# Kernel optimization log

Hardware: AMD Instinct MI355X
Metric: run time of the kernel (lower is better)

Reference implementation:

```python
import jax, jax.numpy as jnp
import numpy as np

N = 50000   # nodes
E = 800000  # edges
D = 128     # nin (= edge_dim)
H = 8       # heads
C = 16      # out_channels per head (nout // nhead)
EPS = 1e-16


def setup_inputs() -> dict:
    key = jax.random.key(0)
    ks = jax.random.split(key, 12)
    s = 1.0 / np.sqrt(D)
    inp = {
        "x": jax.random.normal(ks[0], (N, D), dtype=jnp.float32),
        "edge_attr": jax.random.normal(ks[1], (E, D), dtype=jnp.float32),
        "Wq": jax.random.normal(ks[2], (D, H * C), dtype=jnp.float32) * s,
        "bq": jnp.zeros((H * C,), dtype=jnp.float32),
        "Wk": jax.random.normal(ks[3], (D, H * C), dtype=jnp.float32) * s,
        "bk": jnp.zeros((H * C,), dtype=jnp.float32),
        "Wv": jax.random.normal(ks[4], (D, H * C), dtype=jnp.float32) * s,
        "bv": jnp.zeros((H * C,), dtype=jnp.float32),
        "We": jax.random.normal(ks[5], (D, H * C), dtype=jnp.float32) * s,  # lin_edge, bias=False
        "Wskip": jax.random.normal(ks[6], (D, H * C), dtype=jnp.float32) * s,
        "bskip": jnp.zeros((H * C,), dtype=jnp.float32),
        "edge_index": jax.random.randint(ks[7], (2, E), 0, N, dtype=jnp.int64),
    }
    return inp


def reference(x, edge_attr, Wq, bq, Wk, bk, Wv, bv, We, Wskip, bskip, edge_index):
    src = edge_index[0]  # j (message source)
    dst = edge_index[1]  # i (message target)

    q = (x @ Wq + bq).reshape(N, H, C)           # per-node query
    k = (x @ Wk + bk).reshape(N, H, C)           # per-node key
    v = (x @ Wv + bv).reshape(N, H, C)           # per-node value
    e = (edge_attr @ We).reshape(E, H, C)        # per-edge projection

    q_i = q[dst]                                  # [E, H, C]
    k_j = k[src] + e
    v_j = v[src] + e

    alpha = jnp.einsum("ehc,ehc->eh", q_i, k_j) / np.sqrt(C)  # [E, H]

    # segment softmax over edges grouped by destination node
    m = jax.ops.segment_max(alpha, dst, num_segments=N)        # [N, H]
    m = jnp.where(jnp.isfinite(m), m, 0.0)
    p = jnp.exp(alpha - m[dst])                                # [E, H]
    denom = jax.ops.segment_sum(p, dst, num_segments=N)        # [N, H]
    attn = p / (denom[dst] + EPS)                              # [E, H]

    msg = attn[:, :, None] * v_j                               # [E, H, C]
    out = jax.ops.segment_sum(msg, dst, num_segments=N)        # [N, H, C]
    out = out.reshape(N, H * C)

    # root weight (skip connection)
    out = out + x @ Wskip + bskip
    return out
```

## Files before the change

kernel.cpp:

```cpp
#include <hip/hip_runtime.h>

typedef __attribute__((ext_vector_type(4))) float  f32x4;
typedef __attribute__((ext_vector_type(8))) short  s16x8;

__device__ __forceinline__ short f2bf(float f) {
    unsigned u = __builtin_bit_cast(unsigned, f);
    u += 0x7FFFu + ((u >> 16) & 1u);
    return (short)(u >> 16);
}
__device__ __forceinline__ float bf2f(short s) {
    unsigned u = ((unsigned)(unsigned short)s) << 16;
    return __builtin_bit_cast(float, u);
}

__device__ __forceinline__ void atomic_pk_add_bf16(void* addr, unsigned data) {
    asm volatile("global_atomic_pk_add_bf16 %0, %1, off"
                 :: "v"(addr), "v"(data) : "memory");
}

#define DEPTH 128
#define HEADS 8
#define TILE_M 64

#define LOAD_BFRAG(bfrag, Wt, wc, lane)                                         \
    _Pragma("unroll") for (int nt_ = 0; nt_ < 4; nt_++)                         \
    _Pragma("unroll") for (int kk_ = 0; kk_ < 4; kk_++) {                       \
        int col_ = (wc) + nt_ * 16 + ((lane) & 15);                             \
        int kidx_ = kk_ * 32 + ((lane) >> 4) * 8;                               \
        bfrag[nt_][kk_] = *(const s16x8*)&(Wt)[col_ * 128 + kidx_];             \
    }

__global__ void prep_w(const float* __restrict__ Wq, const float* __restrict__ Wk,
                       const float* __restrict__ Wv, const float* __restrict__ We,
                       const float* __restrict__ Wsk, short* __restrict__ Wt5) {
    int idx = blockIdx.x * 256 + threadIdx.x;
    if (idx >= 5 * DEPTH * DEPTH) return;
    int mat = idx >> 14;
    int rem = idx & 16383;
    int k = rem >> 7, c = rem & 127;
    const float* W = (mat == 0) ? Wq : (mat == 1) ? Wk : (mat == 2) ? Wv : (mat == 3) ? We : Wsk;
    Wt5[mat * 16384 + c * 128 + k] = f2bf(W[k * 128 + c]);
}

__global__ __launch_bounds__(512, 1) void node_proj(
    const float* __restrict__ x, const short* __restrict__ Wt5,
    const float* __restrict__ bq, const float* __restrict__ bk,
    const float* __restrict__ bv, const float* __restrict__ bsk,
    short* __restrict__ qb, short* __restrict__ kb, short* __restrict__ vb,
    float* __restrict__ skb, int Nn) {
    __shared__ short Asm[TILE_M][136];
    int tid = threadIdx.x, wave = tid >> 6, lane = tid & 63;
    int row0 = blockIdx.x * TILE_M;

    for (int i_ = 0; i_ < 4; i_++) {
        int f_ = tid + i_ * 512;
        int r_ = f_ >> 5, c4_ = f_ & 31;
        int gr_ = row0 + r_;
        float4 v_ = (gr_ < Nn) ? ((const float4*)x)[(size_t)gr_ * 32 + c4_]
                               : make_float4(0.f, 0.f, 0.f, 0.f);
        short* d_ = &Asm[r_][c4_ * 4];
        d_[0] = f2bf(v_.x); d_[1] = f2bf(v_.y); d_[2] = f2bf(v_.z); d_[3] = f2bf(v_.w);
    }
    __syncthreads();

    int wr = (wave >> 1) * 16, wc = (wave & 1) * 64;

    for (int mat = 0; mat < 4; mat++) {
        const short* Wt = Wt5 + ((mat < 3) ? mat : 4) * 16384;
        const float* bias = (mat == 0) ? bq : (mat == 1) ? bk : (mat == 2) ? bv : bsk;
        s16x8 bfrag[4][4];
        LOAD_BFRAG(bfrag, Wt, wc, lane);
        f32x4 acc[4];
#pragma unroll
        for (int nt = 0; nt < 4; nt++) acc[nt] = (f32x4){0.f, 0.f, 0.f, 0.f};
#pragma unroll
        for (int kk = 0; kk < 4; kk++) {
            s16x8 a = *(const s16x8*)&Asm[wr + (lane & 15)][kk * 32 + (lane >> 4) * 8];
#pragma unroll
            for (int nt = 0; nt < 4; nt++)
                acc[nt] = __builtin_amdgcn_mfma_f32_16x16x32_bf16(a, bfrag[nt][kk], acc[nt], 0, 0, 0);
        }
#pragma unroll
        for (int nt = 0; nt < 4; nt++) {
            int col = wc + nt * 16 + (lane & 15);
            float b = bias[col];
#pragma unroll
            for (int i = 0; i < 4; i++) {
                int row = row0 + wr + (lane >> 4) * 4 + i;
                if (row < Nn) {
                    float val = acc[nt][i] + b;
                    if (mat == 0)      qb[(size_t)row * 128 + col] = f2bf(val);
                    else if (mat == 1) kb[(size_t)row * 128 + col] = f2bf(val);
                    else if (mat == 2) vb[(size_t)row * 128 + col] = f2bf(val);
                    else               skb[(size_t)row * 128 + col] = val;
                }
            }
        }
    }
}

__global__ __launch_bounds__(512) void fused_edge_stream(
    const float* __restrict__ ea, const short* __restrict__ Wt5,
    const short* __restrict__ qb, const short* __restrict__ kb,
    const short* __restrict__ vb, const int* __restrict__ eidx,
    short* __restrict__ outacc, float* __restrict__ denom, int Ee) {
    const short* Wt = Wt5 + 3 * 16384;

    __shared__ short Asm[TILE_M][136];
    __shared__ short Es[TILE_M][136];
    __shared__ float Pls[TILE_M][HEADS];
    __shared__ int Ss[TILE_M], Ds[TILE_M];

    int tid = threadIdx.x, wave = tid >> 6, lane = tid & 63;
    int e0 = blockIdx.x * TILE_M;
    int cnt = Ee - e0; if (cnt > TILE_M) cnt = TILE_M;

    if (tid < TILE_M) {
        int ge = e0 + tid;
        Ss[tid] = (tid < cnt) ? eidx[ge] : 0;
        Ds[tid] = (tid < cnt) ? eidx[Ee + ge] : -1;
    }
    {
        float4 fl[4];
#pragma unroll
        for (int i_ = 0; i_ < 4; i_++) {
            int f_ = tid + i_ * 512;
            int r_ = f_ >> 5, c4_ = f_ & 31;
            fl[i_] = make_float4(0.f, 0.f, 0.f, 0.f);
            if (r_ < cnt)
                fl[i_] = ((const float4*)ea)[(size_t)(e0 + r_) * 32 + c4_];
        }
#pragma unroll
        for (int i_ = 0; i_ < 4; i_++) {
            int f_ = tid + i_ * 512;
            int r_ = f_ >> 5, c4_ = f_ & 31;
            short4 pkd;
            pkd.x = f2bf(fl[i_].x); pkd.y = f2bf(fl[i_].y);
            pkd.z = f2bf(fl[i_].z); pkd.w = f2bf(fl[i_].w);
            *(short4*)&Asm[r_][c4_ * 4] = pkd;
        }
    }
    __syncthreads();

    int wr = (wave >> 1) * 16, wc = (wave & 1) * 64;
    {
        s16x8 bfrag[4][4];
        LOAD_BFRAG(bfrag, Wt, wc, lane);
        f32x4 acc[4];
#pragma unroll
        for (int nt = 0; nt < 4; nt++) acc[nt] = (f32x4){0.f, 0.f, 0.f, 0.f};
#pragma unroll
        for (int kk = 0; kk < 4; kk++) {
            s16x8 a = *(const s16x8*)&Asm[wr + (lane & 15)][kk * 32 + (lane >> 4) * 8];
#pragma unroll
            for (int nt = 0; nt < 4; nt++)
                acc[nt] = __builtin_amdgcn_mfma_f32_16x16x32_bf16(a, bfrag[nt][kk], acc[nt], 0, 0, 0);
        }
#pragma unroll
        for (int nt = 0; nt < 4; nt++) {
            int col = wc + nt * 16 + (lane & 15);
#pragma unroll
            for (int i = 0; i < 4; i++)
                Es[wr + (lane >> 4) * 4 + i][col] = f2bf(acc[nt][i]);
        }
    }
    __syncthreads();

    {
        int eL = tid >> 3, h = tid & 7;
        if (eL < cnt) {
            int src = Ss[eL], dst = Ds[eL];
            const short* qp = &qb[(size_t)dst * 128 + h * 16];
            const short* kp = &kb[(size_t)src * 128 + h * 16];
            s16x8 q0 = *(const s16x8*)qp, q1 = *(const s16x8*)(qp + 8);
            s16x8 k0 = *(const s16x8*)kp, k1 = *(const s16x8*)(kp + 8);
            s16x8 ev0 = *(const s16x8*)&Es[eL][h * 16];
            s16x8 ev1 = *(const s16x8*)&Es[eL][h * 16 + 8];
            float a_val = 0.f;
#pragma unroll
            for (int c = 0; c < 8; c++) {
                a_val += bf2f(q0[c]) * (bf2f(k0[c]) + bf2f(ev0[c]));
                a_val += bf2f(q1[c]) * (bf2f(k1[c]) + bf2f(ev1[c]));
            }
            Pls[eL][h] = __expf(fminf(a_val * 0.25f, 60.f));
        }
    }
    __syncthreads();

    {
        int base = wave * 8;
        int h = lane >> 3;
        unsigned vvr[8];
        int dr[8];
#pragma unroll
        for (int k = 0; k < 8; k++) {
            int eL = base + k;
            bool ok = (eL < cnt);
            int src = ok ? Ss[eL] : 0;
            dr[k] = ok ? Ds[eL] : -1;
            vvr[k] = *(const unsigned*)&vb[(size_t)src * 128 + lane * 2];
        }
#pragma unroll
        for (int k = 0; k < 8; k++) {
            int d = dr[k];
            if (d < 0) continue;
            int eL = base + k;
            float p = Pls[eL][h];
            unsigned vv = vvr[k];
            unsigned ee = *(const unsigned*)&Es[eL][lane * 2];
            float c0 = p * (bf2f((short)(vv & 0xffff)) + bf2f((short)(ee & 0xffff)));
            float c1 = p * (bf2f((short)(vv >> 16))    + bf2f((short)(ee >> 16)));
            unsigned pkd = (unsigned)(unsigned short)f2bf(c0) |
                           ((unsigned)(unsigned short)f2bf(c1) << 16);
            atomic_pk_add_bf16(&outacc[(size_t)d * 128 + lane * 2], pkd);
            if ((lane & 7) == 0) atomicAdd(&denom[(size_t)d * HEADS + h], p);
        }
    }
}

__global__ void finalize(const short* __restrict__ outacc, const float* __restrict__ denom,
                         const float* __restrict__ skb, float* __restrict__ out, int total4) {
    int idx = blockIdx.x * 256 + threadIdx.x;
    if (idx >= total4) return;
    int n = idx >> 5, q4 = idx & 31;
    int h = q4 >> 2;
    float inv = 1.f / (denom[(size_t)n * HEADS + h] + 1e-16f);
    uint2 a = ((const uint2*)outacc)[idx];
    float4 sk = ((const float4*)skb)[idx];
    float4 r;
    r.x = bf2f((short)(a.x & 0xffff)) * inv + sk.x;
    r.y = bf2f((short)(a.x >> 16))    * inv + sk.y;
    r.z = bf2f((short)(a.y & 0xffff)) * inv + sk.z;
    r.w = bf2f((short)(a.y >> 16))    * inv + sk.w;
    ((float4*)out)[idx] = r;
}

extern "C" void kernel_launch(void* const* d_in, const int* in_sizes, int n_in,
                              void* d_out, int out_size, void* d_ws, size_t ws_size,
                              hipStream_t stream) {
    const float* x   = (const float*)d_in[0];
    const float* ea  = (const float*)d_in[1];
    const float* Wq  = (const float*)d_in[2];
    const float* bq  = (const float*)d_in[3];
    const float* Wk  = (const float*)d_in[4];
    const float* bk  = (const float*)d_in[5];
    const float* Wv  = (const float*)d_in[6];
    const float* bv  = (const float*)d_in[7];
    const float* We  = (const float*)d_in[8];
    const float* Wsk = (const float*)d_in[9];
    const float* bsk = (const float*)d_in[10];
    const int*   eidx = (const int*)d_in[11];

    int Nn = in_sizes[0] / 128;
    int Ee = in_sizes[1] / 128;
    float* out = (float*)d_out;

    size_t need = 0;
    size_t off_qb  = need; need += (size_t)Nn * 128 * 2;
    size_t off_kb  = need; need += (size_t)Nn * 128 * 2;
    size_t off_vb  = need; need += (size_t)Nn * 128 * 2;
    size_t off_skb = need; need += (size_t)Nn * 128 * 4;
    size_t off_oa  = need; need += (size_t)Nn * 128 * 2;
    size_t off_dn  = need; need += (size_t)Nn * HEADS * 4;
    size_t off_wt  = need; need += 5 * 16384 * 2;
    (void)need;

    char* ws = (char*)d_ws;
    short* qb    = (short*)(ws + off_qb);
    short* kb    = (short*)(ws + off_kb);
    short* vb    = (short*)(ws + off_vb);
    float* skb   = (float*)(ws + off_skb);
    short* outacc= (short*)(ws + off_oa);
    float* denom = (float*)(ws + off_dn);
    short* Wt5   = (short*)(ws + off_wt);

    hipMemsetAsync(outacc, 0, (size_t)Nn * 128 * 2 + (size_t)Nn * HEADS * 4, stream);

    prep_w<<<(5 * 16384 + 255) / 256, 256, 0, stream>>>(Wq, Wk, Wv, We, Wsk, Wt5);
    node_proj<<<(Nn + TILE_M - 1) / TILE_M, 512, 0, stream>>>(
        x, Wt5, bq, bk, bv, bsk, qb, kb, vb, skb, Nn);
    fused_edge_stream<<<(Ee + TILE_M - 1) / TILE_M, 512, 0, stream>>>(
        ea, Wt5, qb, kb, vb, eidx, outacc, denom, Ee);
    finalize<<<(Nn * 32 + 255) / 256, 256, 0, stream>>>(
        outacc, denom, skb, out, Nn * 32);
}
```

Baseline: 388.3 us.

## Halve edge-kernel block to 256 threads and alias A/E shared tiles

The fused edge kernel now runs 4 waves per 64-edge tile instead of 8. Each wave computes a full 16x128 edge-projection row strip in two column halves, reusing its A fragments, and writes the result over the same LDS buffer that held the bf16 edge_attr tile. Halving the threads and dropping one LDS tile is meant to fit more blocks per CU and hide gather and atomic latency. In exchange each thread issues twice the loads, score computations and atomics, and register pressure rises from the 16-entry gather arrays and the repeated B-fragment loads.

```diff
diff --git a/kernel.cpp b/kernel.cpp
--- a/kernel.cpp
+++ b/kernel.cpp
@@ -99,15 +99,14 @@
     }
 }
 
-__global__ __launch_bounds__(512) void fused_edge_stream(
+__global__ __launch_bounds__(256) void fused_edge_stream(
     const float* __restrict__ ea, const short* __restrict__ Wt5,
     const short* __restrict__ qb, const short* __restrict__ kb,
     const short* __restrict__ vb, const int* __restrict__ eidx,
     short* __restrict__ outacc, float* __restrict__ denom, int Ee) {
     const short* Wt = Wt5 + 3 * 16384;
 
-    __shared__ short Asm[TILE_M][136];
-    __shared__ short Es[TILE_M][136];
+    __shared__ short U[TILE_M][136];
     __shared__ float Pls[TILE_M][HEADS];
     __shared__ int Ss[TILE_M], Ds[TILE_M];
 
@@ -121,79 +120,105 @@
         Ds[tid] = (tid < cnt) ? eidx[Ee + ge] : -1;
     }
     {
-        float4 fl[4];
-#pragma unroll
-        for (int i_ = 0; i_ < 4; i_++) {
-            int f_ = tid + i_ * 512;
+        float4 fl[8];
+#pragma unroll
+        for (int i_ = 0; i_ < 8; i_++) {
+            int f_ = tid + i_ * 256;
             int r_ = f_ >> 5, c4_ = f_ & 31;
             fl[i_] = make_float4(0.f, 0.f, 0.f, 0.f);
             if (r_ < cnt)
                 fl[i_] = ((const float4*)ea)[(size_t)(e0 + r_) * 32 + c4_];
         }
 #pragma unroll
-        for (int i_ = 0; i_ < 4; i_++) {
-            int f_ = tid + i_ * 512;
+        for (int i_ = 0; i_ < 8; i_++) {
+            int f_ = tid + i_ * 256;
             int r_ = f_ >> 5, c4_ = f_ & 31;
             short4 pkd;
             pkd.x = f2bf(fl[i_].x); pkd.y = f2bf(fl[i_].y);
             pkd.z = f2bf(fl[i_].z); pkd.w = f2bf(fl[i_].w);
-            *(short4*)&Asm[r_][c4_ * 4] = pkd;
+            *(short4*)&U[r_][c4_ * 4] = pkd;
         }
     }
     __syncthreads();
 
-    int wr = (wave >> 1) * 16, wc = (wave & 1) * 64;
+    int wr = wave * 16;
     {
-        s16x8 bfrag[4][4];
-        LOAD_BFRAG(bfrag, Wt, wc, lane);
-        f32x4 acc[4];
-#pragma unroll
-        for (int nt = 0; nt < 4; nt++) acc[nt] = (f32x4){0.f, 0.f, 0.f, 0.f};
-#pragma unroll
-        for (int kk = 0; kk < 4; kk++) {
-            s16x8 a = *(const s16x8*)&Asm[wr + (lane & 15)][kk * 32 + (lane >> 4) * 8];
-#pragma unroll
-            for (int nt = 0; nt < 4; nt++)
-                acc[nt] = __builtin_amdgcn_mfma_f32_16x16x32_bf16(a, bfrag[nt][kk], acc[nt], 0, 0, 0);
-        }
-#pragma unroll
-        for (int nt = 0; nt < 4; nt++) {
-            int col = wc + nt * 16 + (lane & 15);
-#pragma unroll
-            for (int i = 0; i < 4; i++)
-                Es[wr + (lane >> 4) * 4 + i][col] = f2bf(acc[nt][i]);
+        s16x8 afr[4];
+#pragma unroll
+        for (int kk = 0; kk < 4; kk++)
+            afr[kk] = *(const s16x8*)&U[wr + (lane & 15)][kk * 32 + (lane >> 4) * 8];
+#pragma unroll
+        for (int half = 0; half < 2; half++) {
+            int wc = half * 64;
+            s16x8 bfrag[4][4];
+            LOAD_BFRAG(bfrag, Wt, wc, lane);
+            f32x4 acc[4];
+#pragma unroll
+            for (int nt = 0; nt < 4; nt++) acc[nt] = (f32x4){0.f, 0.f, 0.f, 0.f};
+#pragma unroll
+            for (int kk = 0; kk < 4; kk++)
+#pragma unroll
+                for (int nt = 0; nt < 4; nt++)
+                    acc[nt] = __builtin_amdgcn_mfma_f32_16x16x32_bf16(
+                        afr[kk], bfrag[nt][kk], acc[nt], 0, 0, 0);
+#pragma unroll
+            for (int nt = 0; nt < 4; nt++) {
+                int col = wc + nt * 16 + (lane & 15);
+#pragma unroll
+                for (int i = 0; i < 4; i++)
+                    U[wr + (lane >> 4) * 4 + i][col] = f2bf(acc[nt][i]);
+            }
         }
     }
     __syncthreads();
 
     {
-        int eL = tid >> 3, h = tid & 7;
-        if (eL < cnt) {
-            int src = Ss[eL], dst = Ds[eL];
-            const short* qp = &qb[(size_t)dst * 128 + h * 16];
-            const short* kp = &kb[(size_t)src * 128 + h * 16];
-            s16x8 q0 = *(const s16x8*)qp, q1 = *(const s16x8*)(qp + 8);
-            s16x8 k0 = *(const s16x8*)kp, k1 = *(const s16x8*)(kp + 8);
-            s16x8 ev0 = *(const s16x8*)&Es[eL][h * 16];
-            s16x8 ev1 = *(const s16x8*)&Es[eL][h * 16 + 8];
+        int eL0 = tid >> 3, h = tid & 7;
+        int eL1 = eL0 + 32;
+        bool ok0 = (eL0 < cnt), ok1 = (eL1 < cnt);
+        int s0 = ok0 ? Ss[eL0] : 0, d0 = ok0 ? Ds[eL0] : 0;
+        int s1 = ok1 ? Ss[eL1] : 0, d1 = ok1 ? Ds[eL1] : 0;
+        const short* qp0 = &qb[(size_t)d0 * 128 + h * 16];
+        const short* kp0 = &kb[(size_t)s0 * 128 + h * 16];
+        const short* qp1 = &qb[(size_t)d1 * 128 + h * 16];
+        const short* kp1 = &kb[(size_t)s1 * 128 + h * 16];
+        s16x8 q00 = *(const s16x8*)qp0, q01 = *(const s16x8*)(qp0 + 8);
+        s16x8 k00 = *(const s16x8*)kp0, k01 = *(const s16x8*)(kp0 + 8);
+        s16x8 q10 = *(const s16x8*)qp1, q11 = *(const s16x8*)(qp1 + 8);
+        s16x8 k10 = *(const s16x8*)kp1, k11 = *(const s16x8*)(kp1 + 8);
+
+        if (ok0) {
+            s16x8 ev0 = *(const s16x8*)&U[eL0][h * 16];
+            s16x8 ev1 = *(const s16x8*)&U[eL0][h * 16 + 8];
             float a_val = 0.f;
 #pragma unroll
             for (int c = 0; c < 8; c++) {
-                a_val += bf2f(q0[c]) * (bf2f(k0[c]) + bf2f(ev0[c]));
-                a_val += bf2f(q1[c]) * (bf2f(k1[c]) + bf2f(ev1[c]));
+                a_val += bf2f(q00[c]) * (bf2f(k00[c]) + bf2f(ev0[c]));
+                a_val += bf2f(q01[c]) * (bf2f(k01[c]) + bf2f(ev1[c]));
             }
-            Pls[eL][h] = __expf(fminf(a_val * 0.25f, 60.f));
+            Pls[eL0][h] = __expf(fminf(a_val * 0.25f, 60.f));
+        }
+        if (ok1) {
+            s16x8 ev0 = *(const s16x8*)&U[eL1][h * 16];
+            s16x8 ev1 = *(const s16x8*)&U[eL1][h * 16 + 8];
+            float a_val = 0.f;
+#pragma unroll
+            for (int c = 0; c < 8; c++) {
+                a_val += bf2f(q10[c]) * (bf2f(k10[c]) + bf2f(ev0[c]));
+                a_val += bf2f(q11[c]) * (bf2f(k11[c]) + bf2f(ev1[c]));
+            }
+            Pls[eL1][h] = __expf(fminf(a_val * 0.25f, 60.f));
         }
     }
     __syncthreads();
 
     {
-        int base = wave * 8;
+        int base = wave * 16;
         int h = lane >> 3;
-        unsigned vvr[8];
-        int dr[8];
-#pragma unroll
-        for (int k = 0; k < 8; k++) {
+        unsigned vvr[16];
+        int dr[16];
+#pragma unroll
+        for (int k = 0; k < 16; k++) {
             int eL = base + k;
             bool ok = (eL < cnt);
             int src = ok ? Ss[eL] : 0;
@@ -201,13 +226,13 @@
             vvr[k] = *(const unsigned*)&vb[(size_t)src * 128 + lane * 2];
         }
 #pragma unroll
-        for (int k = 0; k < 8; k++) {
+        for (int k = 0; k < 16; k++) {
             int d = dr[k];
             if (d < 0) continue;
             int eL = base + k;
             float p = Pls[eL][h];
             unsigned vv = vvr[k];
-            unsigned ee = *(const unsigned*)&Es[eL][lane * 2];
+            unsigned ee = *(const unsigned*)&U[eL][lane * 2];
             float c0 = p * (bf2f((short)(vv & 0xffff)) + bf2f((short)(ee & 0xffff)));
             float c1 = p * (bf2f((short)(vv >> 16))    + bf2f((short)(ee >> 16)));
             unsigned pkd = (unsigned)(unsigned short)f2bf(c0) |
@@ -279,7 +304,7 @@
     prep_w<<<(5 * 16384 + 255) / 256, 256, 0, stream>>>(Wq, Wk, Wv, We, Wsk, Wt5);
     node_proj<<<(Nn + TILE_M - 1) / TILE_M, 512, 0, stream>>>(
         x, Wt5, bq, bk, bv, bsk, qb, kb, vb, skb, Nn);
-    fused_edge_stream<<<(Ee + TILE_M - 1) / TILE_M, 512, 0, stream>>>(
+    fused_edge_stream<<<(Ee + TILE_M - 1) / TILE_M, 256, 0, stream>>>(
         ea, Wt5, qb, kb, vb, eidx, outacc, denom, Ee);
     finalize<<<(Nn * 32 + 255) / 256, 256, 0, stream>>>(
         outacc, denom, skb, out, Nn * 32);
```

Result: faster. 378.9 us (-2.4%).
